# Kernel optimization log

Hardware: AMD Instinct MI355X
Metric: run time of the kernel (lower is better)

Reference implementation:

```python
import jax, jax.numpy as jnp
import numpy as np

B, S, D = 4, 2048, 1024

def setup_inputs() -> dict:
    key = jax.random.key(0)
    k1, k2, k3, k4 = jax.random.split(key, 4)
    scale = 1.0 / np.sqrt(D)
    x = jax.random.normal(k1, (B, S, D), dtype=jnp.float32)
    Wq = jax.random.normal(k2, (D, D), dtype=jnp.float32) * scale
    Wk = jax.random.normal(k3, (D, D), dtype=jnp.float32) * scale
    Wv = jax.random.normal(k4, (D, D), dtype=jnp.float32) * scale
    return {"x": x, "Wq": Wq, "Wk": Wk, "Wv": Wv}

def reference(x, Wq, Wk, Wv):
    # Linear projections (nn.Linear with bias=False computes x @ W.T)
    q = jnp.einsum('bsd,ed->bse', x, Wq)
    k = jnp.einsum('bsd,ed->bse', x, Wk)
    v = jnp.einsum('bsd,ed->bse', x, Wv)
    # HRR binding: circular convolution of k and v == elementwise product in FFT domain
    fq = jnp.fft.fft(q, axis=-1)
    fk = jnp.fft.fft(k, axis=-1)
    fv = jnp.fft.fft(v, axis=-1)
    # Causal associative memory: cumulative sum of bound key-value pairs over sequence
    mem = jnp.cumsum(fk * fv, axis=-2)  # [B, S, D] complex
    # Unbind with query via approximate inverse (complex conjugate of fft(q))
    out = jnp.fft.ifft(mem * jnp.conj(fq), axis=-1).real
    return out.astype(x.dtype)
```

## Files before the change

kernel.cpp:

```cpp
#include <hip/hip_runtime.h>

#define BB 4
#define SS 2048
#define DD 1024
#define MM 8192
#define CH 64
#define RR 32
#define PI_F 3.14159265358979323846f

typedef __attribute__((ext_vector_type(8))) short bf16x8;
typedef __attribute__((ext_vector_type(4))) float f32x4;

__device__ __forceinline__ unsigned short f2bf(float f) {
  unsigned int u = __float_as_uint(f);
  u = (u + 0x7FFFu + ((u >> 16) & 1u)) >> 16;
  return (unsigned short)u;
}
__device__ __forceinline__ float bf2f(unsigned short h) {
  return __uint_as_float(((unsigned int)h) << 16);
}

__global__ __launch_bounds__(256) void convert_bf16(
    const float* __restrict__ src, unsigned short* __restrict__ dst) {
  const long i = ((long)blockIdx.x * 256 + threadIdx.x) * 4;
  const float4 v = *(const float4*)&src[i];
  ushort4 o;
  o.x = f2bf(v.x); o.y = f2bf(v.y); o.z = f2bf(v.z); o.w = f2bf(v.w);
  *(ushort4*)&dst[i] = o;
}

__global__ __launch_bounds__(256) void convert_w(
    const float* __restrict__ Wq, const float* __restrict__ Wk,
    const float* __restrict__ Wv, unsigned short* __restrict__ dst) {
  const int z = blockIdx.y;
  const float* src = (z == 0) ? Wq : (z == 1) ? Wk : Wv;
  const long i = ((long)blockIdx.x * 256 + threadIdx.x) * 4;
  const float4 v = *(const float4*)&src[i];
  ushort4 o;
  o.x = f2bf(v.x); o.y = f2bf(v.y); o.z = f2bf(v.z); o.w = f2bf(v.w);
  *(ushort4*)&dst[(size_t)z * DD * DD + i] = o;
}

__device__ __forceinline__ void async16(const void* g, void* l) {
  __builtin_amdgcn_global_load_lds(
      (const __attribute__((address_space(1))) void*)g,
      (__attribute__((address_space(3))) void*)l, 16, 0, 0);
}

#define GW(n)  asm volatile("s_waitcnt vmcnt(" #n ")" ::: "memory")
#define BAR()  asm volatile("s_barrier" ::: "memory")
#define SB0()  __builtin_amdgcn_sched_barrier(0)

#define STA(buf, i, T) async16(xb + (size_t)(m0 + 64 * (i)) * DD + (T) * 64 + aOff, \
                               &Als[(buf) * 16384 + (i) * 4096 + slot8])
#define STB(buf, p, T) async16(W + (size_t)(n0 + 16 * (p)) * DD + (T) * 64 + bOff, \
                               &Bls[(buf) * 16384 + (p) * 4096 + slot8])
#define LDA(buf) { _Pragma("unroll") for (int mt = 0; mt < 8; ++mt) { \
    af[mt][0] = *(const bf16x8*)&Als[(buf) * 16384 + aRd + mt * 1024 + qoff0]; \
    af[mt][1] = *(const bf16x8*)&Als[(buf) * 16384 + aRd + mt * 1024 + qoff1]; } }
#define LDB(buf, p, bank) { \
    bank[0] = *(const bf16x8*)&Bls[(buf) * 16384 + (p) * 4096 + bRd + qoff0]; \
    bank[1] = *(const bf16x8*)&Bls[(buf) * 16384 + (p) * 4096 + bRd + qoff1]; }
#define MMA(p, bank) { __builtin_amdgcn_s_setprio(1); \
    _Pragma("unroll") for (int mt = 0; mt < 8; ++mt) { \
      acc[mt][p] = __builtin_amdgcn_mfma_f32_16x16x32_bf16(af[mt][0], bank[0], acc[mt][p], 0, 0, 0); \
      acc[mt][p] = __builtin_amdgcn_mfma_f32_16x16x32_bf16(af[mt][1], bank[1], acc[mt][p], 0, 0, 0); } \
    __builtin_amdgcn_s_setprio(0); }

__global__ __launch_bounds__(512, 2) void gemm_mfma(
    const unsigned short* __restrict__ xb,
    const unsigned short* __restrict__ Wb,
    float* __restrict__ outq, unsigned short* __restrict__ KV) {
  const int z = blockIdx.z;
  const unsigned short* W = Wb + (size_t)z * DD * DD;

  __shared__ unsigned short Als[2 * 16384];
  __shared__ unsigned short Bls[2 * 16384];

  const int tid  = threadIdx.x;
  const int lane = tid & 63;
  const int w    = tid >> 6;
  const int wm   = w >> 2;
  const int gq   = w & 3;
  const int fr   = lane & 15;
  const int kq   = lane >> 4;

  const int m0 = blockIdx.x * 256;
  const int n0 = blockIdx.y * 256;

  const int slot  = tid;
  const int srow  = slot >> 3;
  const int sq    = (slot & 7) ^ (srow & 7);
  const int slot8 = slot * 8;
  const size_t aOff = (size_t)srow * DD + sq * 8;
  const size_t bOff = (size_t)(64 * (slot >> 7) + ((slot >> 3) & 15)) * DD + sq * 8;

  const int qoff0 = ((0 + kq) ^ (fr & 7)) * 8;
  const int qoff1 = ((4 + kq) ^ (fr & 7)) * 8;
  const int aRd = wm * 8192 + fr * 64;
  const int bRd = gq * 1024 + fr * 64;

  f32x4 acc[8][4] = {};
  bf16x8 af[8][2];
  bf16x8 bva[2], bvb[2];

  STA(0, 0, 0); STA(0, 1, 0); STA(0, 2, 0); STA(0, 3, 0);
  STB(0, 0, 0); STB(0, 1, 0); STB(0, 2, 0); STB(0, 3, 0);
  STA(1, 0, 1); STA(1, 1, 1); STB(1, 0, 1); STB(1, 1, 1);

  for (int T = 0; T < 14; ++T) {
    const int buf = T & 1;
    SB0(); GW(4); BAR();
    LDB(buf, 0, bva);
    LDA(buf);
    LDB(buf, 1, bvb);
    STB(buf ^ 1, 2, T + 1); STB(buf ^ 1, 3, T + 1);
    STA(buf ^ 1, 2, T + 1); STA(buf ^ 1, 3, T + 1);
    MMA(0, bva);
    MMA(1, bvb);
    SB0(); BAR();
    LDB(buf, 2, bva);
    LDB(buf, 3, bvb);
    STA(buf, 0, T + 2); STA(buf, 1, T + 2);
    STB(buf, 0, T + 2); STB(buf, 1, T + 2);
    MMA(2, bva);
    MMA(3, bvb);
  }
  SB0(); GW(4); BAR();
  LDB(0, 0, bva); LDA(0); LDB(0, 1, bvb);
  STB(1, 2, 15); STB(1, 3, 15); STA(1, 2, 15); STA(1, 3, 15);
  MMA(0, bva); MMA(1, bvb);
  SB0(); BAR();
  LDB(0, 2, bva); LDB(0, 3, bvb);
  MMA(2, bva); MMA(3, bvb);
  SB0(); GW(0); BAR();
  LDB(1, 0, bva); LDA(1); LDB(1, 1, bvb);
  MMA(0, bva); MMA(1, bvb);
  SB0(); BAR();
  LDB(1, 2, bva); LDB(1, 3, bvb);
  MMA(2, bva); MMA(3, bvb);

  const int col = lane & 15;
  const int r0  = (lane >> 4) * 4;
  const int mBase = m0 + wm * 128;
  const int nBase = n0 + gq * 64;
  if (z == 0) {
    #pragma unroll
    for (int mt = 0; mt < 8; ++mt)
      #pragma unroll
      for (int p = 0; p < 4; ++p)
        #pragma unroll
        for (int r = 0; r < 4; ++r)
          outq[(size_t)(mBase + mt * 16 + r0 + r) * DD + nBase + p * 16 + col] =
              acc[mt][p][r];
  } else {
    unsigned short* Ck = KV + (size_t)(z - 1) * DD;
    #pragma unroll
    for (int mt = 0; mt < 8; ++mt)
      #pragma unroll
      for (int p = 0; p < 4; ++p)
        #pragma unroll
        for (int r = 0; r < 4; ++r)
          Ck[(size_t)(mBase + mt * 16 + r0 + r) * 2048 + nBase + p * 16 + col] =
              f2bf(acc[mt][p][r]);
  }
}

__device__ __forceinline__ int pidx(int i) { return i + (i >> 6); }
#define BUFSZ 1040
__device__ __forceinline__ int pidx16(int i) { return i + (i >> 4); }
#define MEMSZ 546

__device__ __forceinline__ int rev4(int p) {
  unsigned r = __brev((unsigned)p) >> 22;
  return (int)(((r & 0x155u) << 1) | ((r & 0x2AAu) >> 1));
}

__host__ __device__ constexpr int clog2(int s) {
  return (s == 256) ? 8 : (s == 64) ? 6 : (s == 16) ? 4 : (s == 4) ? 2 : 0;
}

template <int S>
__device__ __forceinline__ void fwd_stage(float2 x[4], int t) {
  float c1 = 1.0f, s1 = 0.0f;
  if (S > 1) {
    const int j = t & (S - 1);
    __sincosf(-2.0f * PI_F * (float)j / (float)(4 * S), &s1, &c1);
  }
  const float c2 = c1 * c1 - s1 * s1, s2 = 2.0f * c1 * s1;
  const float c3 = c1 * c2 - s1 * s2, s3 = c1 * s2 + s1 * c2;
  const float Ar = x[0].x + x[2].x, Ai = x[0].y + x[2].y;
  const float Br = x[1].x + x[3].x, Bi = x[1].y + x[3].y;
  const float Cr = x[0].x - x[2].x, Ci = x[0].y - x[2].y;
  const float dr = x[1].x - x[3].x, di = x[1].y - x[3].y;
  const float y1r = Cr + di, y1i = Ci - dr;
  const float y2r = Ar - Br, y2i = Ai - Bi;
  const float y3r = Cr - di, y3i = Ci + dr;
  x[0] = make_float2(Ar + Br, Ai + Bi);
  x[1] = make_float2(y1r * c1 - y1i * s1, y1r * s1 + y1i * c1);
  x[2] = make_float2(y2r * c2 - y2i * s2, y2r * s2 + y2i * c2);
  x[3] = make_float2(y3r * c3 - y3i * s3, y3r * s3 + y3i * c3);
}

template <int S>
__device__ __forceinline__ void inv_stage(float2 x[4], int t) {
  float c1 = 1.0f, s1 = 0.0f;
  if (S > 1) {
    const int j = t & (S - 1);
    __sincosf(2.0f * PI_F * (float)j / (float)(4 * S), &s1, &c1);
  }
  const float c2 = c1 * c1 - s1 * s1, s2 = 2.0f * c1 * s1;
  const float c3 = c1 * c2 - s1 * s2, s3 = c1 * s2 + s1 * c2;
  const float u0r = x[0].x,                   u0i = x[0].y;
  const float u1r = x[1].x * c1 - x[1].y * s1, u1i = x[1].x * s1 + x[1].y * c1;
  const float u2r = x[2].x * c2 - x[2].y * s2, u2i = x[2].x * s2 + x[2].y * c2;
  const float u3r = x[3].x * c3 - x[3].y * s3, u3i = x[3].x * s3 + x[3].y * c3;
  const float Er = u0r + u2r, Ei = u0i + u2i;
  const float Fr = u0r - u2r, Fi = u0i - u2i;
  const float Gr = u1r + u3r, Gi = u1i + u3i;
  const float Hr = u1r - u3r, Hi = u1i - u3i;
  x[0] = make_float2(Er + Gr, Ei + Gi);
  x[1] = make_float2(Fr - Hi, Fi + Hr);
  x[2] = make_float2(Er - Gr, Ei - Gi);
  x[3] = make_float2(Fr + Hi, Fi - Hr);
}

template <int SW, int SR>
__device__ __forceinline__ void xchg(float2* buf, float2 x[4], int t) {
  constexpr int LW2 = clog2(SW), LR = clog2(SR);
  #pragma unroll
  for (int n = 0; n < 4; ++n)
    buf[pidx(((t >> LW2) << (LW2 + 2)) + (t & (SW - 1)) + n * SW)] = x[n];
  __syncthreads();
  #pragma unroll
  for (int n = 0; n < 4; ++n)
    x[n] = buf[pidx(((t >> LR) << (LR + 2)) + (t & (SR - 1)) + n * SR)];
  __syncthreads();
}

__device__ __forceinline__ void fwd_fft(float2* buf, float2 x[4], int t) {
  fwd_stage<256>(x, t); xchg<256, 64>(buf, x, t);
  fwd_stage<64>(x, t);  xchg<64, 16>(buf, x, t);
  fwd_stage<16>(x, t);  xchg<16, 4>(buf, x, t);
  fwd_stage<4>(x, t);   xchg<4, 1>(buf, x, t);
  fwd_stage<1>(x, t);
  #pragma unroll
  for (int n = 0; n < 4; ++n) buf[pidx(4 * t + n)] = x[n];
  __syncthreads();
}

__global__ __launch_bounds__(256) void bind_kernel(unsigned short* __restrict__ KV) {
  __shared__ float2 buf[BUFSZ];
  const int t = threadIdx.x;
  unsigned short* row = KV + (long)blockIdx.x * 2048;

  float2 x[4];
  #pragma unroll
  for (int n = 0; n < 4; ++n) {
    const int i = t + 256 * n;
    x[n] = make_float2(bf2f(row[i]), bf2f(row[1024 + i]));
  }
  fwd_fft(buf, x, t);

  float2* Prow = (float2*)row;
  #pragma unroll
  for (int m = 0; m < 2; ++m) {
    const int s = t + 256 * m;
    if (s == 0) {
      const float2 W0   = buf[pidx(0)];
      const float2 W512 = buf[pidx(2)];
      Prow[0] = make_float2(W0.x * W0.y, W512.x * W512.y);
    } else {
      const int p1 = rev4(s);
      const int p2 = rev4(1024 - s);
      const float2 F1 = buf[pidx(p1)], F2 = buf[pidx(p2)];
      const float fkr = 0.5f * (F1.x + F2.x), fki = 0.5f * (F1.y - F2.y);
      const float fvr = 0.5f * (F1.y + F2.y), fvi = 0.5f * (F2.x - F1.x);
      Prow[s] = make_float2(fkr * fvr - fki * fvi, fkr * fvi + fki * fvr);
    }
  }
}

__global__ __launch_bounds__(256) void scan_chunk_sum(
    const float2* __restrict__ P, float2* __restrict__ csum) {
  const int chunk = blockIdx.x;
  const int batch = blockIdx.y >> 1;
  const int f = (blockIdx.y & 1) * 256 + threadIdx.x;
  long base = ((long)batch * SS + (long)chunk * RR) * 512 + f;
  float sr = 0.0f, si = 0.0f;
  #pragma unroll
  for (int i0 = 0; i0 < RR; i0 += 8) {
    float2 p[8];
    #pragma unroll
    for (int j = 0; j < 8; ++j) p[j] = P[base + (long)(i0 + j) * 512];
    #pragma unroll
    for (int j = 0; j < 8; ++j) { sr += p[j].x; si += p[j].y; }
  }
  csum[((long)batch * CH + chunk) * 512 + f] = make_float2(sr, si);
}

__global__ __launch_bounds__(256) void scan_chunk_scan(float2* csum) {
  const int idx = blockIdx.x * 256 + threadIdx.x;
  const int batch = idx >> 9;
  const int f = idx & 511;
  float2 v[CH];
  #pragma unroll
  for (int c = 0; c < CH; ++c) v[c] = csum[((long)batch * CH + c) * 512 + f];
  float rr = 0.0f, ri = 0.0f;
  #pragma unroll
  for (int c = 0; c < CH; ++c) {
    const float2 x = v[c];
    csum[((long)batch * CH + c) * 512 + f] = make_float2(rr, ri);
    rr += x.x; ri += x.y;
  }
}

__global__ __launch_bounds__(256) void scan_apply(
    float2* __restrict__ P, const float2* __restrict__ csum) {
  const int chunk = blockIdx.x;
  const int batch = blockIdx.y >> 1;
  const int f = (blockIdx.y & 1) * 256 + threadIdx.x;
  float2 off = csum[((long)batch * CH + chunk) * 512 + f];
  float ar = off.x, ai = off.y;
  long base = ((long)batch * SS + (long)chunk * RR) * 512 + f;
  #pragma unroll
  for (int i0 = 0; i0 < RR; i0 += 8) {
    float2 p[8];
    #pragma unroll
    for (int j = 0; j < 8; ++j) p[j] = P[base + (long)(i0 + j) * 512];
    #pragma unroll
    for (int j = 0; j < 8; ++j) {
      ar += p[j].x; ai += p[j].y;
      P[base + (long)(i0 + j) * 512] = make_float2(ar, ai);
    }
  }
}

__global__ __launch_bounds__(256) void unbind_kernel(
    float* __restrict__ qout, const float2* __restrict__ mem) {
  __shared__ float2 buf[BUFSZ];
  __shared__ float2 m0s[MEMSZ], m1s[MEMSZ];
  const int t = threadIdx.x;
  const long r0 = (long)blockIdx.x * 2;
  float* row0 = qout + r0 * DD;
  float* row1 = row0 + DD;
  const float2* mem0 = mem + r0 * 512;
  const float2* mem1 = mem0 + 512;

  float2 x[4];
  #pragma unroll
  for (int n = 0; n < 4; ++n) {
    const int i = t + 256 * n;
    x[n] = make_float2(row0[i], row1[i]);
  }
  #pragma unroll
  for (int n = 0; n < 2; ++n) {
    const int s = t + 256 * n;
    const float2 a = mem0[s], b = mem1[s];
    if (s == 0) {
      m0s[pidx16(0)]   = make_float2(a.x, 0.0f);
      m0s[pidx16(512)] = make_float2(a.y, 0.0f);
      m1s[pidx16(0)]   = make_float2(b.x, 0.0f);
      m1s[pidx16(512)] = make_float2(b.y, 0.0f);
    } else {
      m0s[pidx16(s)] = a;
      m1s[pidx16(s)] = b;
    }
  }
  fwd_fft(buf, x, t);

  float2 z[4];
  #pragma unroll
  for (int m = 0; m < 4; ++m) {
    const int p   = t + 256 * m;
    const int bin = rev4(p);
    const int p2  = rev4((1024 - bin) & 1023);
    const float2 F1 = buf[pidx(p)], F2 = buf[pidx(p2)];
    const float q0r = 0.5f * (F1.x + F2.x), q0i = 0.5f * (F1.y - F2.y);
    const float q1r = 0.5f * (F1.y + F2.y), q1i = 0.5f * (F2.x - F1.x);
    const int  ix = (bin <= 512) ? bin : 1024 - bin;
    const float sg = (bin <= 512) ? 1.0f : -1.0f;
    float2 m0 = m0s[pidx16(ix)], m1 = m1s[pidx16(ix)];
    m0.y *= sg; m1.y *= sg;
    const float z0r = m0.x * q0r + m0.y * q0i, z0i = m0.y * q0r - m0.x * q0i;
    const float z1r = m1.x * q1r + m1.y * q1i, z1i = m1.y * q1r - m1.x * q1i;
    z[m] = make_float2(z0r - z1i, z0i + z1r);
  }
  __syncthreads();
  #pragma unroll
  for (int m = 0; m < 4; ++m) buf[pidx(t + 256 * m)] = z[m];
  __syncthreads();
  #pragma unroll
  for (int n = 0; n < 4; ++n) x[n] = buf[pidx(4 * t + n)];

  inv_stage<1>(x, t);   xchg<1, 4>(buf, x, t);
  inv_stage<4>(x, t);   xchg<4, 16>(buf, x, t);
  inv_stage<16>(x, t);  xchg<16, 64>(buf, x, t);
  inv_stage<64>(x, t);  xchg<64, 256>(buf, x, t);
  inv_stage<256>(x, t);

  const float sc = 1.0f / 1024.0f;
  #pragma unroll
  for (int n = 0; n < 4; ++n) {
    const int i = t + 256 * n;
    row0[i] = x[n].x * sc;
    row1[i] = x[n].y * sc;
  }
}

extern "C" void kernel_launch(void* const* d_in, const int* in_sizes, int n_in,
                              void* d_out, int out_size, void* d_ws, size_t ws_size,
                              hipStream_t stream) {
  (void)in_sizes; (void)n_in; (void)out_size;
  const float* x  = (const float*)d_in[0];
  const float* Wq = (const float*)d_in[1];
  const float* Wk = (const float*)d_in[2];
  const float* Wv = (const float*)d_in[3];
  float* out = (float*)d_out;

  const size_t wbytes = (size_t)3 * DD * DD * 2;
  auto need = [&](size_t MHr, size_t nB) {
    return wbytes + MHr * DD * 2 + MHr * 4096 + nB * CH * 512 * 8;
  };
  const int nPass = (ws_size >= need(8192, 4)) ? 1 : 2;
  const size_t MH = MM / nPass;
  const int    nB = BB / nPass;

  char* ws = (char*)d_ws;
  unsigned short* Wb = (unsigned short*)ws;
  unsigned short* xb = (unsigned short*)(ws + wbytes);
  unsigned short* KV = (unsigned short*)(ws + wbytes + MH * DD * 2);
  float2*       csum = (float2*)((char*)KV + MH * 4096);

  convert_w<<<dim3(DD * DD / 1024, 3), 256, 0, stream>>>(Wq, Wk, Wv, Wb);

  for (int h = 0; h < nPass; ++h) {
    const float* xh   = x   + (size_t)h * MH * DD;
    float*       outh = out + (size_t)h * MH * DD;

    convert_bf16<<<MH * DD / 1024, 256, 0, stream>>>(xh, xb);
    gemm_mfma<<<dim3(MH / 256, DD / 256, 3), dim3(512), 0, stream>>>(xb, Wb, outh, KV);
    bind_kernel<<<MH, 256, 0, stream>>>(KV);
    scan_chunk_sum<<<dim3(CH, nB * 2), 256, 0, stream>>>((const float2*)KV, csum);
    scan_chunk_scan<<<nB * 2, 256, 0, stream>>>(csum);
    scan_apply<<<dim3(CH, nB * 2), 256, 0, stream>>>((float2*)KV, csum);
    unbind_kernel<<<MH / 2, 256, 0, stream>>>(outh, (const float2*)KV);
  }
}
```

Measured before the change: 228.7 us.

## Restructure GEMM main loop into four-phase schedule with finer-grained LDS loads

Splits each K-step of the bf16 MFMA GEMM into four sub-phases, each loading half the A fragments and all four B fragments into separate registers. Asynchronous global-to-LDS stores are interleaved between the phases with explicit vmcnt/lgkmcnt waits and barriers. The aim is to overlap LDS reads and global prefetch with MFMA work and reduce stalls at each barrier. It adds many more barriers per iteration, uses more B-fragment registers, and depends on hand-tuned wait counts being correct.

```diff
diff --git a/kernel.cpp b/kernel.cpp
--- a/kernel.cpp
+++ b/kernel.cpp
@@ -48,6 +48,9 @@
 }
 
 #define GW(n)  asm volatile("s_waitcnt vmcnt(" #n ")" ::: "memory")
+#define LK8()  asm volatile("s_waitcnt lgkmcnt(8)" ::: "memory")
+#define LW()   do { asm volatile("s_waitcnt lgkmcnt(0)" ::: "memory"); \
+                    __builtin_amdgcn_sched_barrier(0); } while (0)
 #define BAR()  asm volatile("s_barrier" ::: "memory")
 #define SB0()  __builtin_amdgcn_sched_barrier(0)
 
@@ -55,16 +58,19 @@
                                &Als[(buf) * 16384 + (i) * 4096 + slot8])
 #define STB(buf, p, T) async16(W + (size_t)(n0 + 16 * (p)) * DD + (T) * 64 + bOff, \
                                &Bls[(buf) * 16384 + (p) * 4096 + slot8])
-#define LDA(buf) { _Pragma("unroll") for (int mt = 0; mt < 8; ++mt) { \
-    af[mt][0] = *(const bf16x8*)&Als[(buf) * 16384 + aRd + mt * 1024 + qoff0]; \
-    af[mt][1] = *(const bf16x8*)&Als[(buf) * 16384 + aRd + mt * 1024 + qoff1]; } }
+
+#define LDAH(buf, mh) { _Pragma("unroll") for (int mt = 0; mt < 4; ++mt) { \
+    const int m_ = (mh) * 4 + mt; \
+    af[m_][0] = *(const bf16x8*)&Als[(buf) * 16384 + aRd + m_ * 1024 + qoff0]; \
+    af[m_][1] = *(const bf16x8*)&Als[(buf) * 16384 + aRd + m_ * 1024 + qoff1]; } }
 #define LDB(buf, p, bank) { \
     bank[0] = *(const bf16x8*)&Bls[(buf) * 16384 + (p) * 4096 + bRd + qoff0]; \
     bank[1] = *(const bf16x8*)&Bls[(buf) * 16384 + (p) * 4096 + bRd + qoff1]; }
-#define MMA(p, bank) { __builtin_amdgcn_s_setprio(1); \
-    _Pragma("unroll") for (int mt = 0; mt < 8; ++mt) { \
-      acc[mt][p] = __builtin_amdgcn_mfma_f32_16x16x32_bf16(af[mt][0], bank[0], acc[mt][p], 0, 0, 0); \
-      acc[mt][p] = __builtin_amdgcn_mfma_f32_16x16x32_bf16(af[mt][1], bank[1], acc[mt][p], 0, 0, 0); } \
+#define MMAQ(mh, nt, bank) { __builtin_amdgcn_s_setprio(1); \
+    _Pragma("unroll") for (int mt = 0; mt < 4; ++mt) { \
+      const int m_ = (mh) * 4 + mt; \
+      acc[m_][nt] = __builtin_amdgcn_mfma_f32_16x16x32_bf16(af[m_][0], bank[0], acc[m_][nt], 0, 0, 0); \
+      acc[m_][nt] = __builtin_amdgcn_mfma_f32_16x16x32_bf16(af[m_][1], bank[1], acc[m_][nt], 0, 0, 0); } \
     __builtin_amdgcn_s_setprio(0); }
 
 __global__ __launch_bounds__(512, 2) void gemm_mfma(
@@ -102,43 +108,66 @@
 
   f32x4 acc[8][4] = {};
   bf16x8 af[8][2];
-  bf16x8 bva[2], bvb[2];
-
-  STA(0, 0, 0); STA(0, 1, 0); STA(0, 2, 0); STA(0, 3, 0);
+  bf16x8 bfv[4][2];
+
   STB(0, 0, 0); STB(0, 1, 0); STB(0, 2, 0); STB(0, 3, 0);
-  STA(1, 0, 1); STA(1, 1, 1); STB(1, 0, 1); STB(1, 1, 1);
+  STA(0, 0, 0); STA(0, 2, 0); STA(0, 1, 0); STA(0, 3, 0);
+  STB(1, 0, 1); STB(1, 1, 1); STB(1, 2, 1); STB(1, 3, 1);
+  STA(1, 0, 1); STA(1, 2, 1);
+  GW(6); BAR();
 
   for (int T = 0; T < 14; ++T) {
     const int buf = T & 1;
-    SB0(); GW(4); BAR();
-    LDB(buf, 0, bva);
-    LDA(buf);
-    LDB(buf, 1, bvb);
-    STB(buf ^ 1, 2, T + 1); STB(buf ^ 1, 3, T + 1);
-    STA(buf ^ 1, 2, T + 1); STA(buf ^ 1, 3, T + 1);
-    MMA(0, bva);
-    MMA(1, bvb);
+    LDB(buf, 0, bfv[0]); LDB(buf, 1, bfv[1]); LDAH(buf, 0);
+    STA(buf ^ 1, 1, T + 1); STA(buf ^ 1, 3, T + 1);
+    LK8(); SB0(); BAR(); LW();
+    MMAQ(0, 0, bfv[0]); MMAQ(0, 1, bfv[1]);
     SB0(); BAR();
-    LDB(buf, 2, bva);
-    LDB(buf, 3, bvb);
-    STA(buf, 0, T + 2); STA(buf, 1, T + 2);
+    LDB(buf, 2, bfv[2]); LDB(buf, 3, bfv[3]);
+    STA(buf, 0, T + 2); STA(buf, 2, T + 2);
+    GW(10); SB0(); BAR(); LW();
+    MMAQ(0, 2, bfv[2]); MMAQ(0, 3, bfv[3]);
+    SB0(); BAR();
+    LDAH(buf, 1);
     STB(buf, 0, T + 2); STB(buf, 1, T + 2);
-    MMA(2, bva);
-    MMA(3, bvb);
-  }
-  SB0(); GW(4); BAR();
-  LDB(0, 0, bva); LDA(0); LDB(0, 1, bvb);
-  STB(1, 2, 15); STB(1, 3, 15); STA(1, 2, 15); STA(1, 3, 15);
-  MMA(0, bva); MMA(1, bvb);
-  SB0(); BAR();
-  LDB(0, 2, bva); LDB(0, 3, bvb);
-  MMA(2, bva); MMA(3, bvb);
-  SB0(); GW(0); BAR();
-  LDB(1, 0, bva); LDA(1); LDB(1, 1, bvb);
-  MMA(0, bva); MMA(1, bvb);
-  SB0(); BAR();
-  LDB(1, 2, bva); LDB(1, 3, bvb);
-  MMA(2, bva); MMA(3, bvb);
+    SB0(); BAR(); LW();
+    MMAQ(1, 0, bfv[0]); MMAQ(1, 1, bfv[1]);
+    SB0(); BAR();
+    STB(buf, 2, T + 2); STB(buf, 3, T + 2);
+    GW(8); SB0(); BAR();
+    MMAQ(1, 2, bfv[2]); MMAQ(1, 3, bfv[3]);
+    SB0(); BAR();
+  }
+
+  LDB(0, 0, bfv[0]); LDB(0, 1, bfv[1]); LDAH(0, 0);
+  STA(1, 1, 15); STA(1, 3, 15);
+  LK8(); SB0(); BAR(); LW();
+  MMAQ(0, 0, bfv[0]); MMAQ(0, 1, bfv[1]);
+  SB0(); BAR();
+  LDB(0, 2, bfv[2]); LDB(0, 3, bfv[3]);
+  GW(8); SB0(); BAR(); LW();
+  MMAQ(0, 2, bfv[2]); MMAQ(0, 3, bfv[3]);
+  SB0(); BAR();
+  LDAH(0, 1);
+  SB0(); BAR(); LW();
+  MMAQ(1, 0, bfv[0]); MMAQ(1, 1, bfv[1]);
+  SB0(); BAR();
+  GW(2); SB0(); BAR();
+  MMAQ(1, 2, bfv[2]); MMAQ(1, 3, bfv[3]);
+  SB0(); BAR();
+  LDB(1, 0, bfv[0]); LDB(1, 1, bfv[1]); LDAH(1, 0);
+  LK8(); SB0(); BAR(); LW();
+  MMAQ(0, 0, bfv[0]); MMAQ(0, 1, bfv[1]);
+  SB0(); BAR();
+  LDB(1, 2, bfv[2]); LDB(1, 3, bfv[3]);
+  GW(0); SB0(); BAR(); LW();
+  MMAQ(0, 2, bfv[2]); MMAQ(0, 3, bfv[3]);
+  SB0(); BAR();
+  LDAH(1, 1);
+  SB0(); BAR(); LW();
+  MMAQ(1, 0, bfv[0]); MMAQ(1, 1, bfv[1]);
+  SB0(); BAR();
+  MMAQ(1, 2, bfv[2]); MMAQ(1, 3, bfv[3]);
 
   const int col = lane & 15;
   const int r0  = (lane >> 4) * 4;
```

New measurement: 241.3 us. 5.5% more time.
